# Kernel optimization log

Hardware: AMD Instinct MI355X
Metric: run time of the kernel (lower is better)

The kernel has to match this reference:

```python
import jax, jax.numpy as jnp
import numpy as np

B, KVH, HPK, D = 4, 8, 4, 128          # batch, n_kv_heads, n_heads_per_kv, head_size
SEQ_KV = 4096                           # cached history length
SEQ = SEQ_KV + 1                        # history + current token
K, LOCAL_K, SINK, RANK = 512, 128, 4, 32


def gather(t, axis, i):
    """Broadcasting take_along_axis, mirroring the torch `gather` helper."""
    axis = axis % t.ndim
    tgt = list(t.shape)
    tgt[axis] = i.shape[axis]
    return jnp.take_along_axis(t, jnp.broadcast_to(i, tgt), axis)


def sparse_q_score(q, key_cpu_t, cur_key_t):
    # q: (B,KVH,HPK,1,D); key_cpu_t: (B,KVH,D,SEQ_KV); cur_key_t: (B,KVH,1,D,1)
    absq = jnp.abs(q).sum(2, keepdims=True)                    # (B,KVH,1,1,D)
    _, idx = jax.lax.top_k(absq, RANK)                         # (B,KVH,1,1,RANK)
    q_proj = gather(q, -1, idx)                                # (B,KVH,HPK,1,RANK)
    idx_t = jnp.swapaxes(idx, -1, -2)                          # (B,KVH,1,RANK,1)
    k_hist = gather(key_cpu_t[:, :, None], -2, idx_t)          # (B,KVH,1,RANK,SEQ_KV)
    k_cur = gather(cur_key_t, -2, idx_t)                       # (B,KVH,1,RANK,1)
    k_proj = jnp.concatenate([k_hist, k_cur], -1)              # (B,KVH,1,RANK,SEQ)
    scale = jnp.sqrt(jnp.abs(q_proj).sum(-1) / jnp.abs(q).sum(-1) * D)[..., None]
    return jnp.matmul(q_proj, k_proj) / scale                  # (B,KVH,HPK,1,SEQ)


def setup_inputs():
    key = jax.random.key(0)
    ks = jax.random.split(key, 6)
    query = jax.random.normal(ks[0], (B, KVH * HPK, 1, D), jnp.float32)
    k = jax.random.normal(ks[1], (B, KVH, 1, D), jnp.float32)
    v = jax.random.normal(ks[2], (B, KVH, 1, D), jnp.float32)
    logmask = jnp.zeros((B, KVH * HPK, 1, SEQ), jnp.float32)
    key_cpu = jax.random.normal(ks[3], (B, KVH, SEQ_KV, D), jnp.float32)
    value_cpu = jax.random.normal(ks[4], (B, KVH, SEQ_KV, D), jnp.float32)
    s_key_cpu = jnp.swapaxes(key_cpu, -1, -2)                  # head-size-contiguous copy
    mean_v = jax.random.normal(ks[5], (B, KVH, 1, 1, D), jnp.float32)
    return {"query": query, "key": k, "value": v, "logmask": logmask,
            "key_cpu": key_cpu, "value_cpu": value_cpu,
            "s_key_cpu": s_key_cpu, "mean_v": mean_v}


def reference(query, key, value, logmask, key_cpu, value_cpu, s_key_cpu, mean_v):
    q = query.reshape(B, KVH, HPK, 1, D)
    k = key.reshape(B, KVH, 1, 1, D)
    v = value.reshape(B, KVH, 1, 1, D)
    lm = logmask.reshape(B, KVH, HPK, 1, SEQ)
    # approximate scores over the full key history + current key
    score = (sparse_q_score(q, s_key_cpu, jnp.swapaxes(k, 3, 4)) + lm).astype(jnp.float32)
    # causal index over history (excluding current token): 0 = most recent unmasked
    neg = jnp.isneginf(lm[..., :-1])
    ci = jnp.where(neg, -1,
                   jnp.cumsum((~neg)[..., ::-1].astype(jnp.int32), -1)[..., ::-1] - 1)
    is_local = (0 <= ci) & (ci < LOCAL_K)
    is_sink = ci >= SEQ - SINK - 1
    fmax = jnp.finfo(jnp.float32).max
    topk_score = jnp.where(is_local | is_sink, fmax, score[..., :-1]).sum(2, keepdims=True)
    kk = min(K + SINK, SEQ)
    _, indices = jax.lax.top_k(topk_score, kk)                 # (B,KVH,1,1,kk)
    # running mean value update
    mean_v_new = (mean_v * (SEQ - 1) + v.astype(jnp.float32)) / SEQ
    # weight reallocation to the mean value
    norm = jax.nn.softmax(score, -1)
    kv_weight = gather(norm, -1, indices).sum(-1) + norm[..., -1]  # (B,KVH,HPK,1)
    # gather selected K/V and append current token
    kv_idx = indices[..., 0, :, None]                          # (B,KVH,1,kk,1)
    key_g = jnp.concatenate([gather(key_cpu[:, :, None], -2, kv_idx), k], -2)   # (B,KVH,1,kk+1,D)
    val_g = jnp.concatenate([gather(value_cpu[:, :, None], -2, kv_idx), v], -2)
    cur_idx = jnp.full(indices.shape[:-1] + (1,), SEQ - 1, indices.dtype)
    lm_g = gather(lm, -1, jnp.concatenate([indices, cur_idx], -1))  # (B,KVH,HPK,1,kk+1)
    # dense attention over the reduced key set
    scores = jnp.matmul(q, jnp.swapaxes(key_g, -1, -2)) * (D ** -0.5) + lm_g
    weights = jax.nn.softmax(scores.astype(jnp.float32), -1) * kv_weight[..., None]
    out = jnp.matmul(weights, val_g) + (1.0 - kv_weight[..., None]) * mean_v_new
    return out.reshape(B, KVH * HPK, 1, D), weights.reshape(B, KVH * HPK, 1, kk + 1)
```

## Files before the change

kernel.cpp:

```cpp
#include <hip/hip_runtime.h>
#include <hip/hip_bf16.h>
#include <math.h>

#define NBH 32
#define HPKN 4
#define DN 128
#define SEQKV 4096
#define SEQN 4097
#define SSTR 4100
#define RANKN 32
#define KSEL 516
#define SINKN 4
#define LOCALK 128
#define NMASK 132
#define NTOP 384
#define NCHUNK 16

__global__ __launch_bounds__(256) void k2_scores(
    const float* __restrict__ q, const float* __restrict__ key,
    const float* __restrict__ skey, const float* __restrict__ lm,
    float* __restrict__ scores, float* __restrict__ tk,
    float2* __restrict__ partials) {
  int bh = blockIdx.y;
  int s0 = blockIdx.x << 8;
  int t = threadIdx.x;
  int wave = t >> 6, lane = t & 63;
  __shared__ float qv[4][128];
  __shared__ float absq[128];
  __shared__ int sel[RANKN];
  __shared__ float qp[4][RANKN];
  __shared__ float wred[4][4];

  {
    float v0 = q[(size_t)bh * 512 + t];
    float v1 = q[(size_t)bh * 512 + 256 + t];
    qv[t >> 7][t & 127] = v0;
    qv[2 + (t >> 7)][t & 127] = v1;
  }
  __syncthreads();
  if (t < 128)
    absq[t] = fabsf(qv[0][t]) + fabsf(qv[1][t]) + fabsf(qv[2][t]) + fabsf(qv[3][t]);
  __syncthreads();
  if (t < 128) {
    float a = absq[t];
    int rank = 0;
    for (int e = 0; e < 128; ++e) {
      float ae = absq[e];
      rank += (ae > a) || (ae == a && e < t);
    }
    if (rank < RANKN) sel[rank] = t;
  }
  __syncthreads();
  {
    float fa = fabsf(qv[wave][lane]) + fabsf(qv[wave][lane + 64]);
    for (int off = 32; off > 0; off >>= 1) fa += __shfl_down(fa, off);
    float full = __shfl(fa, 0);
    float qsel = (lane < RANKN) ? qv[wave][sel[lane]] : 0.f;
    float sv = fabsf(qsel);
    for (int off = 32; off > 0; off >>= 1) sv += __shfl_down(sv, off);
    float selsum = __shfl(sv, 0);
    float scale = sqrtf(selsum / full * 128.f);
    if (lane < RANKN) qp[wave][lane] = qsel / scale;
  }
  __syncthreads();

  if (blockIdx.x == 0) {
    float kv = (lane < RANKN) ? key[bh * 128 + sel[lane]] : 0.f;
    float pr = (lane < RANKN) ? qp[wave][lane] * kv : 0.f;
    for (int off = 32; off > 0; off >>= 1) pr += __shfl_down(pr, off);
    if (lane == 0)
      scores[(size_t)(bh * 4 + wave) * SSTR + SEQKV] =
          pr + lm[(size_t)(bh * 4 + wave) * SEQN + SEQKV];
  }

  const float* kb = skey + (size_t)bh * 128 * 4096;
  float a0 = 0, a1 = 0, a2 = 0, a3 = 0;
#pragma unroll 8
  for (int r = 0; r < RANKN; ++r) {
    float k0 = kb[((size_t)sel[r] << 12) + s0 + t];
    a0 += qp[0][r] * k0;
    a1 += qp[1][r] * k0;
    a2 += qp[2][r] * k0;
    a3 += qp[3][r] * k0;
  }
  float sc[4];
  {
    int s = s0 + t;
    sc[0] = a0 + lm[(size_t)(bh * 4 + 0) * SEQN + s];
    sc[1] = a1 + lm[(size_t)(bh * 4 + 1) * SEQN + s];
    sc[2] = a2 + lm[(size_t)(bh * 4 + 2) * SEQN + s];
    sc[3] = a3 + lm[(size_t)(bh * 4 + 3) * SEQN + s];
    float sum = sc[0] + sc[1] + sc[2] + sc[3];
#pragma unroll
    for (int p = 0; p < 4; ++p)
      scores[(size_t)(bh * 4 + p) * SSTR + s] = sc[p];
    tk[(bh << 12) + s] = sum;
  }

#pragma unroll
  for (int p = 0; p < 4; ++p) {
    float mx = sc[p];
    for (int off = 32; off > 0; off >>= 1) mx = fmaxf(mx, __shfl_down(mx, off));
    if (lane == 0) wred[wave][p] = mx;
  }
  __syncthreads();
  float bm[4];
#pragma unroll
  for (int p = 0; p < 4; ++p)
    bm[p] = fmaxf(fmaxf(wred[0][p], wred[1][p]), fmaxf(wred[2][p], wred[3][p]));
  __syncthreads();
#pragma unroll
  for (int p = 0; p < 4; ++p) {
    float e = expf(sc[p] - bm[p]);
    for (int off = 32; off > 0; off >>= 1) e += __shfl_down(e, off);
    if (lane == 0) wred[wave][p] = e;
  }
  __syncthreads();
  if (t < 4) {
    float s = wred[0][t] + wred[1][t] + wred[2][t] + wred[3][t];
    partials[(size_t)(bh * 4 + t) * NCHUNK + blockIdx.x] = make_float2(bm[t], s);
  }
}

__global__ __launch_bounds__(256) void k3_topk(
    const float* __restrict__ tk, int* __restrict__ indices) {
  int bh = blockIdx.x;
  int t = threadIdx.x;
  int lane = t & 63;
  __shared__ unsigned us[4096];
  __shared__ unsigned hist[2048];
  __shared__ unsigned long long binlist[2048];
  __shared__ unsigned long long selk[512];
  __shared__ unsigned chunkSum[32];
  __shared__ int c1, c2, binB_s, nAbove_s, needed_s;

  {
    const float4* tk4 = (const float4*)(tk + (bh << 12));
    for (int i = t; i < 1024; i += 256) {
      float4 v = tk4[i];
      unsigned b0 = __float_as_uint(v.x), b1 = __float_as_uint(v.y);
      unsigned b2 = __float_as_uint(v.z), b3 = __float_as_uint(v.w);
      us[i * 4 + 0] = (b0 & 0x80000000u) ? ~b0 : (b0 | 0x80000000u);
      us[i * 4 + 1] = (b1 & 0x80000000u) ? ~b1 : (b1 | 0x80000000u);
      us[i * 4 + 2] = (b2 & 0x80000000u) ? ~b2 : (b2 | 0x80000000u);
      us[i * 4 + 3] = (b3 & 0x80000000u) ? ~b3 : (b3 | 0x80000000u);
    }
  }
  for (int i = t; i < 2048; i += 256) hist[i] = 0;
  if (t == 0) { c1 = 0; c2 = 0; }
  __syncthreads();

  for (int s = SINKN + t; s < SEQKV - LOCALK; s += 256)
    atomicAdd(&hist[us[s] >> 21], 1u);
  __syncthreads();

  if (t < 32) {
    unsigned sum = 0;
    for (int i = 0; i < 64; ++i) sum += hist[t * 64 + i];
    chunkSum[t] = sum;
  }
  __syncthreads();

  if (t < 64) {
    int l = t;
    unsigned x = (l < 32) ? chunkSum[l] : 0;
    unsigned sfx = x;
    for (int off = 1; off < 64; off <<= 1) {
      unsigned y = __shfl_down(sfx, off);
      if (l + off < 64) sfx += y;
    }
    unsigned above = sfx - x;
    bool hit = (l < 32) && (above < NTOP) && (above + x >= NTOP);
    unsigned long long mask = __ballot(hit);
    int C = __ffsll(mask) - 1;
    unsigned aboveC = __shfl(above, C);
    unsigned h = hist[C * 64 + l];
    unsigned sfx2 = h;
    for (int off = 1; off < 64; off <<= 1) {
      unsigned y = __shfl_down(sfx2, off);
      if (l + off < 64) sfx2 += y;
    }
    unsigned above2 = aboveC + (sfx2 - h);
    bool hit2 = (above2 < NTOP) && (above2 + h >= NTOP);
    unsigned long long mask2 = __ballot(hit2);
    int lB = __ffsll(mask2) - 1;
    if (l == lB) {
      binB_s = C * 64 + l;
      nAbove_s = (int)above2;
      needed_s = NTOP - (int)above2;
    }
  }
  __syncthreads();
  unsigned B = (unsigned)binB_s;
  int nAbove = nAbove_s, needed = needed_s;

  for (int s0 = SINKN; s0 < SEQKV - LOCALK; s0 += 256) {
    int s = s0 + t;
    bool valid = (s < SEQKV - LOCALK);
    unsigned u = valid ? us[s] : 0u;
    unsigned bin = u >> 21;
    bool win = valid && (bin > B);
    bool bnd = valid && (bin == B);
    unsigned long long mw = __ballot(win);
    unsigned long long mb = __ballot(bnd);
    int bw = 0, bb = 0;
    if (lane == 0) {
      if (mw) bw = atomicAdd(&c1, __popcll(mw));
      if (mb) bb = atomicAdd(&c2, __popcll(mb));
    }
    bw = __shfl(bw, 0);
    bb = __shfl(bb, 0);
    unsigned long long lmask = (1ULL << lane) - 1ULL;
    unsigned long long key = ((unsigned long long)u << 32) | (unsigned)(~s);
    if (win) selk[bw + __popcll(mw & lmask)] = key;
    if (bnd) {
      int pos = bb + __popcll(mb & lmask);
      if (pos < 2048) binlist[pos] = key;
    }
  }
  __syncthreads();
  int m2 = c2;
  int p2 = 1;
  while (p2 < m2) p2 <<= 1;
  for (int i = m2 + t; i < p2; i += 256) binlist[i] = 0ULL;
  __syncthreads();
  for (int k = 2; k <= p2; k <<= 1)
    for (int j = k >> 1; j > 0; j >>= 1) {
      for (int i = t; i < p2; i += 256) {
        int ixj = i ^ j;
        if (ixj > i) {
          bool desc = ((i & k) == 0);
          unsigned long long a = binlist[i], bb2 = binlist[ixj];
          if ((a < bb2) == desc) { binlist[i] = bb2; binlist[ixj] = a; }
        }
      }
      __syncthreads();
    }
  for (int i = t; i < needed; i += 256) selk[nAbove + i] = binlist[i];
  for (int i = NTOP + t; i < 512; i += 256) selk[i] = 0ULL;
  __syncthreads();

  unsigned long long e0 = selk[t], e1 = selk[t + 256];
  int i1 = t + 256;
  for (int k = 2; k <= 512; k <<= 1) {
    for (int j = k >> 1; j > 0; j >>= 1) {
      if (j == 256) {
        if (e0 < e1) { unsigned long long tmp = e0; e0 = e1; e1 = tmp; }
      } else if (j >= 64) {
        selk[t] = e0; selk[i1] = e1;
        __syncthreads();
        unsigned long long p0 = selk[t ^ j], p1 = selk[i1 ^ j];
        __syncthreads();
        bool d0 = ((t & k) == 0), l0 = ((t & j) == 0);
        e0 = (d0 == l0) ? (e0 > p0 ? e0 : p0) : (e0 < p0 ? e0 : p0);
        bool d1 = ((i1 & k) == 0), l1 = ((i1 & j) == 0);
        e1 = (d1 == l1) ? (e1 > p1 ? e1 : p1) : (e1 < p1 ? e1 : p1);
      } else {
        unsigned long long p0 = __shfl_xor(e0, j);
        unsigned long long p1 = __shfl_xor(e1, j);
        bool d0 = ((t & k) == 0), l0 = ((t & j) == 0);
        e0 = (d0 == l0) ? (e0 > p0 ? e0 : p0) : (e0 < p0 ? e0 : p0);
        bool d1 = ((i1 & k) == 0);
        e1 = (d1 == l0) ? (e1 > p1 ? e1 : p1) : (e1 < p1 ? e1 : p1);
      }
    }
  }

  if (t < SINKN) indices[bh * KSEL + t] = t;
  for (int i = t; i < LOCALK; i += 256)
    indices[bh * KSEL + SINKN + i] = (SEQKV - LOCALK) + i;
  indices[bh * KSEL + NMASK + t] = (int)(~(unsigned)(e0 & 0xFFFFFFFFu));
  if (t < NTOP - 256)
    indices[bh * KSEL + NMASK + 256 + t] = (int)(~(unsigned)(e1 & 0xFFFFFFFFu));
}

__global__ __launch_bounds__(256) void k5_qk(
    const float* __restrict__ q, const float* __restrict__ key,
    const float* __restrict__ lm, const float* __restrict__ key_cpu,
    const int* __restrict__ indices, float* __restrict__ s2_g) {
  int bh = blockIdx.y;
  int t = threadIdx.x;
  int wave = t >> 6, lane = t & 63;
  __shared__ float qs[512];
  __shared__ int sidx[KSEL];
  qs[t] = q[((size_t)bh * 4 << 7) + t];
  qs[t + 256] = q[((size_t)bh * 4 << 7) + t + 256];
  for (int j = t; j < KSEL; j += 256) sidx[j] = indices[bh * KSEL + j];
  __syncthreads();

  const float rsqd = 0.08838834764831845f;
  float q0a = qs[lane * 2], q0b = qs[lane * 2 + 1];
  float q1a = qs[128 + lane * 2], q1b = qs[128 + lane * 2 + 1];
  float q2a = qs[256 + lane * 2], q2b = qs[256 + lane * 2 + 1];
  float q3a = qs[384 + lane * 2], q3b = qs[384 + lane * 2 + 1];

  for (int i = 0; i < 5; ++i) {
    int j = (blockIdx.x << 2) + wave + 104 * i;
    if (j > KSEL) continue;
    int sj = (j < KSEL) ? sidx[j] : SEQKV;
    const float* krow = (j < KSEL)
        ? key_cpu + ((((size_t)bh << 12) + sj) << 7)
        : key + ((size_t)bh << 7);
    float2 kk = ((const float2*)krow)[lane];
    float p0 = q0a * kk.x + q0b * kk.y;
    float p1 = q1a * kk.x + q1b * kk.y;
    float p2 = q2a * kk.x + q2b * kk.y;
    float p3 = q3a * kk.x + q3b * kk.y;
    for (int off = 32; off > 0; off >>= 1) {
      p0 += __shfl_down(p0, off);
      p1 += __shfl_down(p1, off);
      p2 += __shfl_down(p2, off);
      p3 += __shfl_down(p3, off);
    }
    if (lane == 0) {
      size_t lmb = (size_t)bh * 4 * SEQN + sj;
      s2_g[(bh * 4 + 0) * 520 + j] = p0 * rsqd + lm[lmb + 0 * SEQN];
      s2_g[(bh * 4 + 1) * 520 + j] = p1 * rsqd + lm[lmb + 1 * SEQN];
      s2_g[(bh * 4 + 2) * 520 + j] = p2 * rsqd + lm[lmb + 2 * SEQN];
      s2_g[(bh * 4 + 3) * 520 + j] = p3 * rsqd + lm[lmb + 3 * SEQN];
    }
  }
}

__global__ __launch_bounds__(256) void k6_stats(
    const float* __restrict__ scores, const float2* __restrict__ partials,
    const int* __restrict__ indices, const float* __restrict__ s2_g,
    const float* __restrict__ value, const float* __restrict__ mean_v,
    float* __restrict__ out_w, float* __restrict__ w_g,
    float* __restrict__ out) {
  int bhp = blockIdx.x;
  int bh = bhp >> 2;
  int t = threadIdx.x;
  __shared__ int sidx[KSEL];
  __shared__ float red[256];
  __shared__ float bc;

  for (int j = t; j < KSEL; j += 256) sidx[j] = indices[bh * KSEL + j];
  __syncthreads();

  const float* srow = scores + (size_t)bhp * SSTR;
  float cur = srow[SEQKV];

  float m = cur, sumexp;
  {
    float2 pc[NCHUNK];
#pragma unroll
    for (int c = 0; c < NCHUNK; ++c) {
      pc[c] = partials[(size_t)bhp * NCHUNK + c];
      m = fmaxf(m, pc[c].x);
    }
    float s = expf(cur - m);
#pragma unroll
    for (int c = 0; c < NCHUNK; ++c) s += pc[c].y * expf(pc[c].x - m);
    sumexp = s;
  }

  float ss = 0.f;
  for (int j = t; j < KSEL; j += 256) ss += expf(srow[sidx[j]] - m);
  red[t] = ss; __syncthreads();
  for (int st = 128; st > 0; st >>= 1) {
    if (t < st) red[t] += red[t + st];
    __syncthreads();
  }
  float kvw;
  if (t == 0) bc = (red[0] + expf(cur - m)) / sumexp;
  __syncthreads();
  kvw = bc; __syncthreads();

  const float* s2r = s2_g + (size_t)bhp * 520;
  float mx2 = -INFINITY;
  for (int j = t; j < KSEL + 1; j += 256) mx2 = fmaxf(mx2, s2r[j]);
  red[t] = mx2; __syncthreads();
  for (int st = 128; st > 0; st >>= 1) {
    if (t < st) red[t] = fmaxf(red[t], red[t + st]);
    __syncthreads();
  }
  float m2 = red[0]; __syncthreads();
  float se2 = 0.f;
  for (int j = t; j < KSEL + 1; j += 256) se2 += expf(s2r[j] - m2);
  red[t] = se2; __syncthreads();
  for (int st = 128; st > 0; st >>= 1) {
    if (t < st) red[t] += red[t + st];
    __syncthreads();
  }
  float inv = kvw / red[0];

  for (int j = t; j < KSEL + 1; j += 256) {
    float w = expf(s2r[j] - m2) * inv;
    out_w[(size_t)bhp * (KSEL + 1) + j] = w;
    w_g[(size_t)bhp * 520 + j] = w;
  }

  if (t < 128) {
    float vcur = value[((size_t)bh << 7) + t];
    float mvn = (mean_v[((size_t)bh << 7) + t] * 4096.f + vcur) / 4097.f;
    out[((size_t)bhp << 7) + t] = (1.f - kvw) * mvn;
  }
}

__global__ __launch_bounds__(256) void k7_wv(
    const float* __restrict__ value, const float* __restrict__ value_cpu,
    const int* __restrict__ indices, const float* __restrict__ w_g,
    float* __restrict__ out) {
  int bh = blockIdx.y;
  int c0 = blockIdx.x << 5;
  int t = threadIdx.x;
  int d = t & 127, half = t >> 7;
  __shared__ int sidx[32];
  __shared__ float wsh[4][32];
  __shared__ float red[2][4][128];

  int nj = min(32, KSEL + 1 - c0);
  if (t < nj) {
    int j = c0 + t;
    sidx[t] = (j < KSEL) ? indices[bh * KSEL + j] : -1;
  }
  if (t < 128) {
    int p = t >> 5, jl = t & 31;
    wsh[p][jl] = (jl < nj) ? w_g[(size_t)(bh * 4 + p) * 520 + c0 + jl] : 0.f;
  }
  __syncthreads();

  float a0 = 0, a1 = 0, a2 = 0, a3 = 0;
  for (int jl = half; jl < nj; jl += 2) {
    int sj = sidx[jl];
    const float* vrow = (sj >= 0)
        ? value_cpu + ((((size_t)bh << 12) + sj) << 7)
        : value + ((size_t)bh << 7);
    float v = vrow[d];
    a0 += wsh[0][jl] * v;
    a1 += wsh[1][jl] * v;
    a2 += wsh[2][jl] * v;
    a3 += wsh[3][jl] * v;
  }
  red[half][0][d] = a0; red[half][1][d] = a1;
  red[half][2][d] = a2; red[half][3][d] = a3;
  __syncthreads();
  if (half == 0) {
#pragma unroll
    for (int p = 0; p < 4; ++p) {
      float s = red[0][p][d] + red[1][p][d];
      atomicAdd(&out[(size_t)(bh * 4 + p) * 128 + d], s);
    }
  }
}

extern "C" void kernel_launch(void* const* d_in, const int* in_sizes, int n_in,
                              void* d_out, int out_size, void* d_ws, size_t ws_size,
                              hipStream_t stream) {
  const float* query     = (const float*)d_in[0];
  const float* key       = (const float*)d_in[1];
  const float* value     = (const float*)d_in[2];
  const float* logmask   = (const float*)d_in[3];
  const float* key_cpu   = (const float*)d_in[4];
  const float* value_cpu = (const float*)d_in[5];
  const float* s_key_cpu = (const float*)d_in[6];
  const float* mean_v    = (const float*)d_in[7];

  float* out   = (float*)d_out;
  float* out_w = out + 16384;

  char* ws = (char*)d_ws;
  int*    indices  = (int*)(ws + 20480);
  float*  scores   = (float*)(ws + 86528);
  float*  tk       = (float*)(ws + 2185728);
  float*  s2_g     = (float*)(ws + 2710016);
  float*  w_g      = (float*)(ws + 2976256);
  float2* partials = (float2*)(ws + 3242496);

  hipLaunchKernelGGL(k2_scores, dim3(NCHUNK, NBH), dim3(256), 0, stream,
                     query, key, s_key_cpu, logmask, scores, tk, partials);
  hipLaunchKernelGGL(k3_topk, dim3(NBH), dim3(256), 0, stream,
                     tk, indices);
  hipLaunchKernelGGL(k5_qk, dim3(26, NBH), dim3(256), 0, stream,
                     query, key, logmask, key_cpu, indices, s2_g);
  hipLaunchKernelGGL(k6_stats, dim3(128), dim3(256), 0, stream,
                     scores, partials, indices, s2_g, value, mean_v,
                     out_w, w_g, out);
  hipLaunchKernelGGL(k7_wv, dim3(17, NBH), dim3(256), 0, stream,
                     value, value_cpu, indices, w_g, out);
}
```

Baseline: 229.2 us.

## Fuse QK, softmax stats and weighted-V tail kernels into one per-head kernel

Replaces the three tail kernels (gathered QK scoring, softmax/kv-weight stats, and weighted value sum with atomics) with a single 512-thread block per batch-head that holds scores and weights in shared memory. This removes two kernel launches, the global round trips through s2_g/w_g, and the atomicAdd accumulation into the output. QK now uses 16-lane groups with float4 loads, and reductions use wave shuffles. In exchange, parallelism drops to 32 blocks, so the gather of 516 value and key rows per head runs on far fewer CUs and may be latency-bound.

```diff
diff --git a/kernel.cpp b/kernel.cpp
--- a/kernel.cpp
+++ b/kernel.cpp
@@ -1,5 +1,4 @@
 #include <hip/hip_runtime.h>
-#include <hip/hip_bf16.h>
 #include <math.h>
 
 #define NBH 32
@@ -274,174 +273,138 @@
     indices[bh * KSEL + NMASK + 256 + t] = (int)(~(unsigned)(e1 & 0xFFFFFFFFu));
 }
 
-__global__ __launch_bounds__(256) void k5_qk(
+__global__ __launch_bounds__(512) void kC_tail(
     const float* __restrict__ q, const float* __restrict__ key,
-    const float* __restrict__ lm, const float* __restrict__ key_cpu,
-    const int* __restrict__ indices, float* __restrict__ s2_g) {
-  int bh = blockIdx.y;
-  int t = threadIdx.x;
-  int wave = t >> 6, lane = t & 63;
-  __shared__ float qs[512];
-  __shared__ int sidx[KSEL];
-  qs[t] = q[((size_t)bh * 4 << 7) + t];
-  qs[t + 256] = q[((size_t)bh * 4 << 7) + t + 256];
-  for (int j = t; j < KSEL; j += 256) sidx[j] = indices[bh * KSEL + j];
-  __syncthreads();
-
-  const float rsqd = 0.08838834764831845f;
-  float q0a = qs[lane * 2], q0b = qs[lane * 2 + 1];
-  float q1a = qs[128 + lane * 2], q1b = qs[128 + lane * 2 + 1];
-  float q2a = qs[256 + lane * 2], q2b = qs[256 + lane * 2 + 1];
-  float q3a = qs[384 + lane * 2], q3b = qs[384 + lane * 2 + 1];
-
-  for (int i = 0; i < 5; ++i) {
-    int j = (blockIdx.x << 2) + wave + 104 * i;
-    if (j > KSEL) continue;
-    int sj = (j < KSEL) ? sidx[j] : SEQKV;
-    const float* krow = (j < KSEL)
-        ? key_cpu + ((((size_t)bh << 12) + sj) << 7)
-        : key + ((size_t)bh << 7);
-    float2 kk = ((const float2*)krow)[lane];
-    float p0 = q0a * kk.x + q0b * kk.y;
-    float p1 = q1a * kk.x + q1b * kk.y;
-    float p2 = q2a * kk.x + q2b * kk.y;
-    float p3 = q3a * kk.x + q3b * kk.y;
-    for (int off = 32; off > 0; off >>= 1) {
-      p0 += __shfl_down(p0, off);
-      p1 += __shfl_down(p1, off);
-      p2 += __shfl_down(p2, off);
-      p3 += __shfl_down(p3, off);
-    }
-    if (lane == 0) {
-      size_t lmb = (size_t)bh * 4 * SEQN + sj;
-      s2_g[(bh * 4 + 0) * 520 + j] = p0 * rsqd + lm[lmb + 0 * SEQN];
-      s2_g[(bh * 4 + 1) * 520 + j] = p1 * rsqd + lm[lmb + 1 * SEQN];
-      s2_g[(bh * 4 + 2) * 520 + j] = p2 * rsqd + lm[lmb + 2 * SEQN];
-      s2_g[(bh * 4 + 3) * 520 + j] = p3 * rsqd + lm[lmb + 3 * SEQN];
-    }
-  }
-}
-
-__global__ __launch_bounds__(256) void k6_stats(
-    const float* __restrict__ scores, const float2* __restrict__ partials,
-    const int* __restrict__ indices, const float* __restrict__ s2_g,
-    const float* __restrict__ value, const float* __restrict__ mean_v,
-    float* __restrict__ out_w, float* __restrict__ w_g,
-    float* __restrict__ out) {
-  int bhp = blockIdx.x;
-  int bh = bhp >> 2;
-  int t = threadIdx.x;
-  __shared__ int sidx[KSEL];
-  __shared__ float red[256];
-  __shared__ float bc;
-
-  for (int j = t; j < KSEL; j += 256) sidx[j] = indices[bh * KSEL + j];
-  __syncthreads();
-
-  const float* srow = scores + (size_t)bhp * SSTR;
-  float cur = srow[SEQKV];
-
-  float m = cur, sumexp;
-  {
-    float2 pc[NCHUNK];
-#pragma unroll
-    for (int c = 0; c < NCHUNK; ++c) {
-      pc[c] = partials[(size_t)bhp * NCHUNK + c];
-      m = fmaxf(m, pc[c].x);
-    }
-    float s = expf(cur - m);
-#pragma unroll
-    for (int c = 0; c < NCHUNK; ++c) s += pc[c].y * expf(pc[c].x - m);
-    sumexp = s;
-  }
-
-  float ss = 0.f;
-  for (int j = t; j < KSEL; j += 256) ss += expf(srow[sidx[j]] - m);
-  red[t] = ss; __syncthreads();
-  for (int st = 128; st > 0; st >>= 1) {
-    if (t < st) red[t] += red[t + st];
+    const float* __restrict__ value, const float* __restrict__ lm,
+    const float* __restrict__ key_cpu, const float* __restrict__ value_cpu,
+    const float* __restrict__ mean_v, const float* __restrict__ scores,
+    const float2* __restrict__ partials, const int* __restrict__ indices,
+    float* __restrict__ out, float* __restrict__ out_w) {
+  const int bh = blockIdx.x;
+  const int t = threadIdx.x;
+  const int wave = t >> 6, lane = t & 63;
+  const int grp = lane >> 4, gl = lane & 15;
+
+  __shared__ int sidxs[520];
+  __shared__ float qv[512];
+  __shared__ float s2s[4 * 520];
+  __shared__ float ws2[4 * 520];
+  __shared__ float redA[8], redB[8], redC[8];
+
+  qv[t] = q[((size_t)bh << 9) + t];
+  for (int j = t; j < KSEL; j += 512) sidxs[j] = indices[bh * KSEL + j];
+  __syncthreads();
+
+  {
+    const float rsqd = 0.08838834764831845f;
+    const float4* qv4 = (const float4*)qv;
+    float4 qA[4], qB[4];
+#pragma unroll
+    for (int p = 0; p < 4; ++p) {
+      qA[p] = qv4[p * 32 + gl * 2];
+      qB[p] = qv4[p * 32 + gl * 2 + 1];
+    }
+    for (int r = 0; r < 17; ++r) {
+      int j = (r << 5) + (wave << 2) + grp;
+      if (j <= KSEL) {
+        int sj = (j < KSEL) ? sidxs[j] : SEQKV;
+        const float* krow = (j < KSEL)
+            ? key_cpu + ((((size_t)bh << 12) + sj) << 7)
+            : key + ((size_t)bh << 7);
+        const float4* k4 = (const float4*)krow;
+        float4 kA = k4[gl * 2], kB = k4[gl * 2 + 1];
+        float d0 = qA[0].x * kA.x + qA[0].y * kA.y + qA[0].z * kA.z + qA[0].w * kA.w +
+                   qB[0].x * kB.x + qB[0].y * kB.y + qB[0].z * kB.z + qB[0].w * kB.w;
+        float d1 = qA[1].x * kA.x + qA[1].y * kA.y + qA[1].z * kA.z + qA[1].w * kA.w +
+                   qB[1].x * kB.x + qB[1].y * kB.y + qB[1].z * kB.z + qB[1].w * kB.w;
+        float d2 = qA[2].x * kA.x + qA[2].y * kA.y + qA[2].z * kA.z + qA[2].w * kA.w +
+                   qB[2].x * kB.x + qB[2].y * kB.y + qB[2].z * kB.z + qB[2].w * kB.w;
+        float d3 = qA[3].x * kA.x + qA[3].y * kA.y + qA[3].z * kA.z + qA[3].w * kA.w +
+                   qB[3].x * kB.x + qB[3].y * kB.y + qB[3].z * kB.z + qB[3].w * kB.w;
+        for (int off = 8; off > 0; off >>= 1) {
+          d0 += __shfl_down(d0, off);
+          d1 += __shfl_down(d1, off);
+          d2 += __shfl_down(d2, off);
+          d3 += __shfl_down(d3, off);
+        }
+        if (gl == 0) {
+          size_t lmb = (size_t)(bh * 4) * SEQN + sj;
+          s2s[0 * 520 + j] = d0 * rsqd + lm[lmb + 0 * SEQN];
+          s2s[1 * 520 + j] = d1 * rsqd + lm[lmb + 1 * SEQN];
+          s2s[2 * 520 + j] = d2 * rsqd + lm[lmb + 2 * SEQN];
+          s2s[3 * 520 + j] = d3 * rsqd + lm[lmb + 3 * SEQN];
+        }
+      }
+    }
+  }
+  __syncthreads();
+
+  const int p = t >> 7, tt = t & 127;
+  const int qw = tt >> 6;
+  const int bhp = bh * 4 + p;
+  float kvw;
+  {
+    const float* srow = scores + (size_t)bhp * SSTR;
+    float cur = srow[SEQKV];
+
+    float m = cur, sumexp;
+    {
+      float2 pc[NCHUNK];
+#pragma unroll
+      for (int c = 0; c < NCHUNK; ++c) {
+        pc[c] = partials[(size_t)bhp * NCHUNK + c];
+        m = fmaxf(m, pc[c].x);
+      }
+      float s = expf(cur - m);
+#pragma unroll
+      for (int c = 0; c < NCHUNK; ++c) s += pc[c].y * expf(pc[c].x - m);
+      sumexp = s;
+    }
+
+    float ss = 0.f;
+    for (int j = tt; j < KSEL; j += 128) ss += expf(srow[sidxs[j]] - m);
+    for (int off = 32; off > 0; off >>= 1) ss += __shfl_down(ss, off);
+    if (lane == 0) redA[p * 2 + qw] = ss;
     __syncthreads();
-  }
-  float kvw;
-  if (t == 0) bc = (red[0] + expf(cur - m)) / sumexp;
-  __syncthreads();
-  kvw = bc; __syncthreads();
-
-  const float* s2r = s2_g + (size_t)bhp * 520;
-  float mx2 = -INFINITY;
-  for (int j = t; j < KSEL + 1; j += 256) mx2 = fmaxf(mx2, s2r[j]);
-  red[t] = mx2; __syncthreads();
-  for (int st = 128; st > 0; st >>= 1) {
-    if (t < st) red[t] = fmaxf(red[t], red[t + st]);
+    float sstot = redA[p * 2] + redA[p * 2 + 1];
+    kvw = (sstot + expf(cur - m)) / sumexp;
+
+    float mx = -INFINITY;
+    for (int j = tt; j < KSEL + 1; j += 128) mx = fmaxf(mx, s2s[p * 520 + j]);
+    for (int off = 32; off > 0; off >>= 1) mx = fmaxf(mx, __shfl_down(mx, off));
+    if (lane == 0) redB[p * 2 + qw] = mx;
     __syncthreads();
-  }
-  float m2 = red[0]; __syncthreads();
-  float se2 = 0.f;
-  for (int j = t; j < KSEL + 1; j += 256) se2 += expf(s2r[j] - m2);
-  red[t] = se2; __syncthreads();
-  for (int st = 128; st > 0; st >>= 1) {
-    if (t < st) red[t] += red[t + st];
+    float m2 = fmaxf(redB[p * 2], redB[p * 2 + 1]);
+    float se = 0.f;
+    for (int j = tt; j < KSEL + 1; j += 128) se += expf(s2s[p * 520 + j] - m2);
+    for (int off = 32; off > 0; off >>= 1) se += __shfl_down(se, off);
+    if (lane == 0) redC[p * 2 + qw] = se;
     __syncthreads();
-  }
-  float inv = kvw / red[0];
-
-  for (int j = t; j < KSEL + 1; j += 256) {
-    float w = expf(s2r[j] - m2) * inv;
-    out_w[(size_t)bhp * (KSEL + 1) + j] = w;
-    w_g[(size_t)bhp * 520 + j] = w;
-  }
-
-  if (t < 128) {
-    float vcur = value[((size_t)bh << 7) + t];
-    float mvn = (mean_v[((size_t)bh << 7) + t] * 4096.f + vcur) / 4097.f;
-    out[((size_t)bhp << 7) + t] = (1.f - kvw) * mvn;
-  }
-}
-
-__global__ __launch_bounds__(256) void k7_wv(
-    const float* __restrict__ value, const float* __restrict__ value_cpu,
-    const int* __restrict__ indices, const float* __restrict__ w_g,
-    float* __restrict__ out) {
-  int bh = blockIdx.y;
-  int c0 = blockIdx.x << 5;
-  int t = threadIdx.x;
-  int d = t & 127, half = t >> 7;
-  __shared__ int sidx[32];
-  __shared__ float wsh[4][32];
-  __shared__ float red[2][4][128];
-
-  int nj = min(32, KSEL + 1 - c0);
-  if (t < nj) {
-    int j = c0 + t;
-    sidx[t] = (j < KSEL) ? indices[bh * KSEL + j] : -1;
-  }
-  if (t < 128) {
-    int p = t >> 5, jl = t & 31;
-    wsh[p][jl] = (jl < nj) ? w_g[(size_t)(bh * 4 + p) * 520 + c0 + jl] : 0.f;
-  }
-  __syncthreads();
-
-  float a0 = 0, a1 = 0, a2 = 0, a3 = 0;
-  for (int jl = half; jl < nj; jl += 2) {
-    int sj = sidx[jl];
-    const float* vrow = (sj >= 0)
-        ? value_cpu + ((((size_t)bh << 12) + sj) << 7)
-        : value + ((size_t)bh << 7);
-    float v = vrow[d];
-    a0 += wsh[0][jl] * v;
-    a1 += wsh[1][jl] * v;
-    a2 += wsh[2][jl] * v;
-    a3 += wsh[3][jl] * v;
-  }
-  red[half][0][d] = a0; red[half][1][d] = a1;
-  red[half][2][d] = a2; red[half][3][d] = a3;
-  __syncthreads();
-  if (half == 0) {
-#pragma unroll
-    for (int p = 0; p < 4; ++p) {
-      float s = red[0][p][d] + red[1][p][d];
-      atomicAdd(&out[(size_t)(bh * 4 + p) * 128 + d], s);
-    }
+    float inv = kvw / (redC[p * 2] + redC[p * 2 + 1]);
+
+    for (int j = tt; j < KSEL + 1; j += 128) {
+      float w = expf(s2s[p * 520 + j] - m2) * inv;
+      ws2[p * 520 + j] = w;
+      out_w[(size_t)bhp * (KSEL + 1) + j] = w;
+    }
+  }
+  __syncthreads();
+
+  {
+    const int d = tt;
+    float vcur = value[((size_t)bh << 7) + d];
+    float mvn = (mean_v[((size_t)bh << 7) + d] * 4096.f + vcur) / 4097.f;
+    float a0 = (1.f - kvw) * mvn, a1 = 0.f, a2 = 0.f, a3 = 0.f;
+    const float* vbase = value_cpu + ((size_t)bh << 19);
+    for (int j = 0; j < KSEL; j += 4) {
+      int s0 = sidxs[j], s1 = sidxs[j + 1], s2i = sidxs[j + 2], s3 = sidxs[j + 3];
+      a0 += ws2[p * 520 + j] * vbase[((size_t)s0 << 7) + d];
+      a1 += ws2[p * 520 + j + 1] * vbase[((size_t)s1 << 7) + d];
+      a2 += ws2[p * 520 + j + 2] * vbase[((size_t)s2i << 7) + d];
+      a3 += ws2[p * 520 + j + 3] * vbase[((size_t)s3 << 7) + d];
+    }
+    a0 += ws2[p * 520 + KSEL] * vcur;
+    out[((size_t)bhp << 7) + d] = (a0 + a1) + (a2 + a3);
   }
 }
 
@@ -464,19 +427,13 @@
   int*    indices  = (int*)(ws + 20480);
   float*  scores   = (float*)(ws + 86528);
   float*  tk       = (float*)(ws + 2185728);
-  float*  s2_g     = (float*)(ws + 2710016);
-  float*  w_g      = (float*)(ws + 2976256);
   float2* partials = (float2*)(ws + 3242496);
 
   hipLaunchKernelGGL(k2_scores, dim3(NCHUNK, NBH), dim3(256), 0, stream,
                      query, key, s_key_cpu, logmask, scores, tk, partials);
   hipLaunchKernelGGL(k3_topk, dim3(NBH), dim3(256), 0, stream,
                      tk, indices);
-  hipLaunchKernelGGL(k5_qk, dim3(26, NBH), dim3(256), 0, stream,
-                     query, key, logmask, key_cpu, indices, s2_g);
-  hipLaunchKernelGGL(k6_stats, dim3(128), dim3(256), 0, stream,
-                     scores, partials, indices, s2_g, value, mean_v,
-                     out_w, w_g, out);
-  hipLaunchKernelGGL(k7_wv, dim3(17, NBH), dim3(256), 0, stream,
-                     value, value_cpu, indices, w_g, out);
+  hipLaunchKernelGGL(kC_tail, dim3(NBH), dim3(512), 0, stream,
+                     query, key, value, logmask, key_cpu, value_cpu,
+                     mean_v, scores, partials, indices, out, out_w);
 }
```

Measured after the change: 258.1 us. +12.6%, slower.
